# Kernel tuning notes

Measured on AMD Instinct MI355X. Metric: run time of the kernel, lower is better.

## Reference

```python
import jax, jax.numpy as jnp
import numpy as np
import math

B, N, C_IN = 4, 512, 32
K = 3            # Chebyshev order -> K+1 polynomial terms
H = 4            # attention heads
OUT_PER_HEAD = 64
ACT_OUT = OUT_PER_HEAD * H  # concat_heads=True


def _prelu(x, a):
    return jnp.where(x >= 0, x, a * x)


def setup_inputs() -> dict:
    key = jax.random.key(0)
    ks = jax.random.split(key, 10)
    stdv = 1.0 / math.sqrt(ACT_OUT)
    inp = {
        "X_real": jax.random.normal(ks[0], (B, N, C_IN), jnp.float32),
        "X_imag": jax.random.normal(ks[1], (B, N, C_IN), jnp.float32),
        "L_real": jax.random.normal(ks[2], (B, K + 1, N, N), jnp.float32),
        "L_imag": jax.random.normal(ks[3], (B, K + 1, N, N), jnp.float32),
        # Chebyshev complex weights, uniform(-stdv, stdv) as in torch init
        "weight_real": jax.random.uniform(ks[4], (K + 1, C_IN, ACT_OUT), jnp.float32, -stdv, stdv),
        "weight_imag": jax.random.uniform(ks[5], (K + 1, C_IN, ACT_OUT), jnp.float32, -stdv, stdv),
        # CVLinear(2*C_IN -> H) complex weight/bias
        "attn_w_real": jax.random.normal(ks[6], (2 * C_IN, H), jnp.float32) * 0.1,
        "attn_w_imag": jax.random.normal(ks[7], (2 * C_IN, H), jnp.float32) * 0.1,
        "attn_b_real": jnp.zeros((H,), jnp.float32),
        "attn_b_imag": jnp.zeros((H,), jnp.float32),
        # CPReLU slopes (PReLU applied to real/imag parts independently)
        "prelu_a_real": jnp.float32(0.25),
        "prelu_a_imag": jnp.float32(0.25),
        "bias_real": jnp.zeros((1, ACT_OUT), jnp.float32),
        "bias_imag": jnp.zeros((1, ACT_OUT), jnp.float32),
    }
    return inp


def reference(X_real, X_imag, L_real, L_imag, weight_real, weight_imag,
              attn_w_real, attn_w_imag, attn_b_real, attn_b_imag,
              prelu_a_real, prelu_a_imag, bias_real, bias_imag):
    C = X_real.shape[-1]
    K1 = weight_real.shape[0]
    # --- attention scores: complex linear on concat([X_i, X_j]) ---
    # split the 2C weight into the X_i half and the X_j half (same math,
    # avoids materializing the B*N*N*2C pairwise concat tensor)
    W1r, W2r = attn_w_real[:C], attn_w_real[C:]
    W1i, W2i = attn_w_imag[:C], attn_w_imag[C:]
    si_re = X_real @ W1r - X_imag @ W1i   # (B,N,H)
    si_im = X_real @ W1i + X_imag @ W1r
    sj_re = X_real @ W2r - X_imag @ W2i
    sj_im = X_real @ W2i + X_imag @ W2r
    # scores[b,i,j,h]
    sc_re = si_re[:, :, None, :] + sj_re[:, None, :, :] + attn_b_real
    sc_im = si_im[:, :, None, :] + sj_im[:, None, :, :] + attn_b_imag
    # CPReLU: PReLU on real/imag independently
    sc_re = _prelu(sc_re, prelu_a_real)
    sc_im = _prelu(sc_im, prelu_a_imag)
    # adjacency mask from |L_real| summed over the K+1 polynomial terms
    mask = (jnp.abs(L_real).sum(axis=1) > 1e-9)[..., None]  # (B,N,N,1)
    NEG = jnp.float32(-1e9)
    re_m = jnp.where(mask, sc_re, NEG)
    im_m = jnp.where(mask, sc_im, NEG)
    attn = jax.nn.softmax(re_m * re_m + im_m * im_m, axis=2)  # softmax over j, (B,N,N,H)
    # --- complex Chebyshev propagation: (L*attn) @ X, per k, per head ---
    lre_xr = jnp.einsum('bknj,bnjh,bjc->bknch', L_real, attn, X_real)
    lim_xi = jnp.einsum('bknj,bnjh,bjc->bknch', L_imag, attn, X_imag)
    lre_xi = jnp.einsum('bknj,bnjh,bjc->bknch', L_real, attn, X_imag)
    lim_xr = jnp.einsum('bknj,bnjh,bjc->bknch', L_imag, attn, X_real)
    LXr = lre_xr - lim_xi
    LXi = lre_xi + lim_xr
    # per-head complex weights: (K+1, C, P, H), out index = p*H + h
    Wr = weight_real.reshape(K1, C, OUT_PER_HEAD, H)
    Wi = weight_imag.reshape(K1, C, OUT_PER_HEAD, H)
    Yre = jnp.einsum('bknch,kcph->bnph', LXr, Wr) - jnp.einsum('bknch,kcph->bnph', LXi, Wi)
    Yim = jnp.einsum('bknch,kcph->bnph', LXr, Wi) + jnp.einsum('bknch,kcph->bnph', LXi, Wr)
    Bsz, Nn = X_real.shape[:2]
    out_re = Yre.reshape(Bsz, Nn, -1) + bias_real
    out_im = Yim.reshape(Bsz, Nn, -1) + bias_imag
    return (out_re, out_im)
```

## Files before the change

kernel.cpp:

```cpp
#include <hip/hip_runtime.h>
#include <hip/hip_bf16.h>

#define BB 4
#define NN 512
#define CC 32
#define KK 4
#define HH 4
#define AOUT 256

#define WS_SI_F   0
#define WS_SII_F  (BB*NN*HH)
#define WS_SJR_F  (2*BB*NN*HH)
#define WS_SJI_F  (3*BB*NN*HH)
#define XT_BASE   131072
#define LX_BASE   393216
#define BRE_BASE  4587520
#define BIM_BASE  4718592

typedef __attribute__((ext_vector_type(8))) short bf16x8;
typedef __attribute__((ext_vector_type(4))) float f32x4;

__device__ __forceinline__ ushort f2bfu(float f){
    union { __hip_bfloat16 h; ushort u; } cv;
    cv.h = __float2bfloat16(f);
    return cv.u;
}
__device__ __forceinline__ short f2bfs(float f){ return (short)f2bfu(f); }
__device__ __forceinline__ float bfu2f(unsigned int u){ return __uint_as_float(u << 16); }

__global__ __launch_bounds__(256) void prep_kernel(
    const float* __restrict__ Xr, const float* __restrict__ Xi,
    const float* __restrict__ AWr, const float* __restrict__ AWi,
    const float* __restrict__ Wr, const float* __restrict__ Wi,
    float* __restrict__ ws, char* __restrict__ wsB)
{
    const int blk = blockIdx.x;
    const int t = threadIdx.x;

    if (blk < 8) {
        int idx = blk*256 + t;
        const float* xr = Xr + (size_t)idx * CC;
        const float* xi = Xi + (size_t)idx * CC;
        float sir[HH] = {0,0,0,0}, sii[HH] = {0,0,0,0};
        float sjr[HH] = {0,0,0,0}, sji[HH] = {0,0,0,0};
        for (int c = 0; c < CC; ++c) {
            float xrc = xr[c], xic = xi[c];
            const float* w1r = AWr + c*HH;
            const float* w1i = AWi + c*HH;
            const float* w2r = AWr + (CC + c)*HH;
            const float* w2i = AWi + (CC + c)*HH;
            #pragma unroll
            for (int h = 0; h < HH; ++h) {
                sir[h] = fmaf(xrc, w1r[h], fmaf(-xic, w1i[h], sir[h]));
                sii[h] = fmaf(xrc, w1i[h], fmaf( xic, w1r[h], sii[h]));
                sjr[h] = fmaf(xrc, w2r[h], fmaf(-xic, w2i[h], sjr[h]));
                sji[h] = fmaf(xrc, w2i[h], fmaf( xic, w2r[h], sji[h]));
            }
        }
        #pragma unroll
        for (int h = 0; h < HH; ++h) {
            ws[WS_SI_F  + idx*HH + h] = sir[h];
            ws[WS_SII_F + idx*HH + h] = sii[h];
            ws[WS_SJR_F + idx*HH + h] = sjr[h];
            ws[WS_SJI_F + idx*HH + h] = sji[h];
        }
    } else if (blk < 40) {
        int bid = (blk - 8)*4 + (t >> 6);
        int part = bid >> 6, b = (bid >> 4) & 3, jb = bid & 15;
        const float* X = part ? Xi : Xr;
        int lane = t & 63;
        int c = lane & 31, jh = lane >> 5;

        unsigned int w[8];
        #pragma unroll
        for (int q = 0; q < 8; ++q) {
            int ji = jh*16 + q*2;
            float f0 = X[((size_t)b*NN + jb*32 + ji  )*CC + c];
            float f1 = X[((size_t)b*NN + jb*32 + ji+1)*CC + c];
            w[q] = (unsigned int)f2bfu(f0) | ((unsigned int)f2bfu(f1) << 16);
        }
        char* tile = wsB + XT_BASE + (((size_t)(part*4 + b)*16 + jb) * 2048);
        uint4* dst = (uint4*)(tile + c*64 + jh*32);
        dst[0] = make_uint4(w[0], w[1], w[2], w[3]);
        dst[1] = make_uint4(w[4], w[5], w[6], w[7]);
    } else {
        int idx = (blk - 40)*256 + t;
        int l  = idx & 63;
        int s  = (idx >> 6) & 7;
        int Nt = (idx >> 9) & 3;
        int h  = idx >> 11;
        int p = Nt*16 + (l & 15), o = p*4 + h;
        int e8 = (l >> 4) * 8;
        unsigned int re_w[4], im_w[4];
        #pragma unroll
        for (int q = 0; q < 4; ++q) {
            unsigned int rw = 0, iw = 0;
            #pragma unroll
            for (int half = 0; half < 2; ++half) {
                int kpos = s*32 + e8 + q*2 + half;
                int ri = kpos >> 7, kk = (kpos >> 5) & 3, c = kpos & 31;
                float wr = Wr[(size_t)(kk*CC + c)*AOUT + o];
                float wi = Wi[(size_t)(kk*CC + c)*AOUT + o];
                unsigned int vre = f2bfu(ri ? -wi : wr);
                unsigned int vim = f2bfu(ri ?  wr : wi);
                rw |= vre << (16*half);
                iw |= vim << (16*half);
            }
            re_w[q] = rw; im_w[q] = iw;
        }
        size_t fo = ((size_t)((h*4 + Nt)*8 + s))*1024 + (size_t)l*16;
        *(uint4*)(wsB + BRE_BASE + fo) = make_uint4(re_w[0], re_w[1], re_w[2], re_w[3]);
        *(uint4*)(wsB + BIM_BASE + fo) = make_uint4(im_w[0], im_w[1], im_w[2], im_w[3]);
    }
}

__global__ __launch_bounds__(128) void cheb_main_kernel(
    const float* __restrict__ Lr_g, const float* __restrict__ Li_g,
    const float* __restrict__ abr, const float* __restrict__ abi,
    const float* __restrict__ par, const float* __restrict__ pai,
    const float* __restrict__ ws, char* __restrict__ wsB)
{
    __shared__ ushort Lf[8][528];
    __shared__ float awf[HH][520];
    __shared__ float wredm[2][HH];
    __shared__ float wreds[2][HH];

    const int bn = blockIdx.x;
    const int b = bn >> 9;
    const int n = bn & (NN - 1);
    const int t = threadIdx.x;
    const int l = t & 63;
    const int w = t >> 6;
    const int jw = 4*t;

    const float4 si_r4 = *(const float4*)(ws + WS_SI_F  + bn*HH);
    const float4 si_i4 = *(const float4*)(ws + WS_SII_F + bn*HH);
    float4 sjr[4], sji[4];
    #pragma unroll
    for (int e = 0; e < 4; ++e) {
        sjr[e] = *(const float4*)(ws + WS_SJR_F + ((size_t)b*NN + jw + e)*HH);
        sji[e] = *(const float4*)(ws + WS_SJI_F + ((size_t)b*NN + jw + e)*HH);
    }
    const float a_r = par[0], a_i = pai[0];

    float am4[4] = {0.f,0.f,0.f,0.f};
    #pragma unroll
    for (int it = 0; it < 8; ++it) {
        const float* src = (it & 4) ? Li_g : Lr_g;
        size_t goff = (((size_t)b*KK + (it & 3))*NN + n)*NN + jw;
        float4 v = *(const float4*)(src + goff);
        if (it < 4) {
            am4[0] += fabsf(v.x); am4[1] += fabsf(v.y);
            am4[2] += fabsf(v.z); am4[3] += fabsf(v.w);
        }
        ushort4 u;
        u.x = f2bfu(v.x); u.y = f2bfu(v.y); u.z = f2bfu(v.z); u.w = f2bfu(v.w);
        *(ushort4*)&Lf[it][jw] = u;
    }

    float sir[HH], sii[HH];
    #pragma unroll
    for (int h = 0; h < HH; ++h) {
        sir[h] = ((const float*)&si_r4)[h] + abr[h];
        sii[h] = ((const float*)&si_i4)[h] + abi[h];
    }
    float v[4][HH];
    float pmax[HH] = {-INFINITY, -INFINITY, -INFINITY, -INFINITY};
    #pragma unroll
    for (int e = 0; e < 4; ++e) {
        bool msk = am4[e] > 1e-9f;
        const float* sjrp = (const float*)&sjr[e];
        const float* sjip = (const float*)&sji[e];
        #pragma unroll
        for (int h = 0; h < HH; ++h) {
            float sr = sir[h] + sjrp[h];
            sr = sr >= 0.f ? sr : a_r * sr;
            float sv = sii[h] + sjip[h];
            sv = sv >= 0.f ? sv : a_i * sv;
            float val;
            if (msk) val = sr*sr + sv*sv;
            else { const float NEG = -1e9f; val = NEG*NEG + NEG*NEG; }
            v[e][h] = val;
            pmax[h] = fmaxf(pmax[h], val);
        }
    }
    #pragma unroll
    for (int h = 0; h < HH; ++h) {
        #pragma unroll
        for (int off = 32; off > 0; off >>= 1)
            pmax[h] = fmaxf(pmax[h], __shfl_xor(pmax[h], off));
    }
    if (l == 0) { wredm[w][0]=pmax[0]; wredm[w][1]=pmax[1]; wredm[w][2]=pmax[2]; wredm[w][3]=pmax[3]; }
    __syncthreads();

    float hm[HH];
    #pragma unroll
    for (int h = 0; h < HH; ++h) hm[h] = fmaxf(wredm[0][h], wredm[1][h]);

    float psum[HH];
    #pragma unroll
    for (int h = 0; h < HH; ++h) {
        float4 ev;
        ev.x = __expf(v[0][h] - hm[h]);
        ev.y = __expf(v[1][h] - hm[h]);
        ev.z = __expf(v[2][h] - hm[h]);
        ev.w = __expf(v[3][h] - hm[h]);
        *(float4*)&awf[h][jw] = ev;
        psum[h] = (ev.x + ev.y) + (ev.z + ev.w);
    }
    #pragma unroll
    for (int h = 0; h < HH; ++h) {
        #pragma unroll
        for (int off = 32; off > 0; off >>= 1)
            psum[h] += __shfl_xor(psum[h], off);
    }
    if (l == 0) { wreds[w][0]=psum[0]; wreds[w][1]=psum[1]; wreds[w][2]=psum[2]; wreds[w][3]=psum[3]; }
    __syncthreads();

    float inv[HH];
    #pragma unroll
    for (int h = 0; h < HH; ++h) inv[h] = 1.0f / (wreds[0][h] + wreds[1][h]);

    const int r_a = l & 15;
    const int jg  = l >> 4;
    const int k_a = r_a >> 2, h_a = r_a & 3;

    f32x4 acc[8];
    #pragma unroll
    for (int a = 0; a < 8; ++a) acc[a] = (f32x4){0.f,0.f,0.f,0.f};

    const char* xtR = wsB + XT_BASE + ((size_t)(0*4 + b)*16 + w*8)*2048;
    const char* xtI = wsB + XT_BASE + ((size_t)(4   + b)*16 + w*8)*2048;
    const int bofs = (l & 15)*64 + jg*16;

#define LOAD_STEP(s, BR0,BR1,BI0,BI1, LR8,LI8, AW0,AW1) do {                  \
        const int j0_ = w*256 + (s)*32 + jg*8;                                \
        BR0 = *(const bf16x8*)(xtR + (s)*2048 +        bofs);                 \
        BR1 = *(const bf16x8*)(xtR + (s)*2048 + 1024 + bofs);                 \
        BI0 = *(const bf16x8*)(xtI + (s)*2048 +        bofs);                 \
        BI1 = *(const bf16x8*)(xtI + (s)*2048 + 1024 + bofs);                 \
        LR8 = *(const bf16x8*)&Lf[k_a][j0_];                                  \
        LI8 = *(const bf16x8*)&Lf[4 + k_a][j0_];                              \
        AW0 = *(const float4*)&awf[h_a][j0_];                                 \
        AW1 = *(const float4*)&awf[h_a][j0_ + 4];                             \
    } while (0)

#define COMP_STEP(BR0,BR1,BI0,BI1, LR8,LI8, AW0,AW1) do {                     \
        float aww_[8];                                                        \
        *(float4*)&aww_[0] = AW0; *(float4*)&aww_[4] = AW1;                   \
        bf16x8 Ar_, Ai_;                                                      \
        _Pragma("unroll")                                                     \
        for (int e_ = 0; e_ < 8; ++e_) {                                      \
            Ar_[e_] = f2bfs(bfu2f((ushort)LR8[e_]) * aww_[e_]);               \
            Ai_[e_] = f2bfs(bfu2f((ushort)LI8[e_]) * aww_[e_]);               \
        }                                                                     \
        acc[0] = __builtin_amdgcn_mfma_f32_16x16x32_bf16(Ar_, BR0, acc[0],0,0,0); \
        acc[1] = __builtin_amdgcn_mfma_f32_16x16x32_bf16(Ar_, BR1, acc[1],0,0,0); \
        acc[2] = __builtin_amdgcn_mfma_f32_16x16x32_bf16(Ai_, BI0, acc[2],0,0,0); \
        acc[3] = __builtin_amdgcn_mfma_f32_16x16x32_bf16(Ai_, BI1, acc[3],0,0,0); \
        acc[4] = __builtin_amdgcn_mfma_f32_16x16x32_bf16(Ar_, BI0, acc[4],0,0,0); \
        acc[5] = __builtin_amdgcn_mfma_f32_16x16x32_bf16(Ar_, BI1, acc[5],0,0,0); \
        acc[6] = __builtin_amdgcn_mfma_f32_16x16x32_bf16(Ai_, BR0, acc[6],0,0,0); \
        acc[7] = __builtin_amdgcn_mfma_f32_16x16x32_bf16(Ai_, BR1, acc[7],0,0,0); \
    } while (0)

    {
        bf16x8 pBr0,pBr1,pBi0,pBi1,pLr,pLi; float4 pA0,pA1;
        bf16x8 qBr0,qBr1,qBi0,qBi1,qLr,qLi; float4 qA0,qA1;
        LOAD_STEP(0, pBr0,pBr1,pBi0,pBi1, pLr,pLi, pA0,pA1);
        LOAD_STEP(1, qBr0,qBr1,qBi0,qBi1, qLr,qLi, qA0,qA1);
        COMP_STEP(pBr0,pBr1,pBi0,pBi1, pLr,pLi, pA0,pA1);
        LOAD_STEP(2, pBr0,pBr1,pBi0,pBi1, pLr,pLi, pA0,pA1);
        COMP_STEP(qBr0,qBr1,qBi0,qBi1, qLr,qLi, qA0,qA1);
        LOAD_STEP(3, qBr0,qBr1,qBi0,qBi1, qLr,qLi, qA0,qA1);
        COMP_STEP(pBr0,pBr1,pBi0,pBi1, pLr,pLi, pA0,pA1);
        LOAD_STEP(4, pBr0,pBr1,pBi0,pBi1, pLr,pLi, pA0,pA1);
        COMP_STEP(qBr0,qBr1,qBi0,qBi1, qLr,qLi, qA0,qA1);
        LOAD_STEP(5, qBr0,qBr1,qBi0,qBi1, qLr,qLi, qA0,qA1);
        COMP_STEP(pBr0,pBr1,pBi0,pBi1, pLr,pLi, pA0,pA1);
        LOAD_STEP(6, pBr0,pBr1,pBi0,pBi1, pLr,pLi, pA0,pA1);
        COMP_STEP(qBr0,qBr1,qBi0,qBi1, qLr,qLi, qA0,qA1);
        LOAD_STEP(7, qBr0,qBr1,qBi0,qBi1, qLr,qLi, qA0,qA1);
        COMP_STEP(pBr0,pBr1,pBi0,pBi1, pLr,pLi, pA0,pA1);
        COMP_STEP(qBr0,qBr1,qBi0,qBi1, qLr,qLi, qA0,qA1);
    }
#undef LOAD_STEP
#undef COMP_STEP

    __syncthreads();

    float* pbuf = &awf[0][0];
    if (w == 1) {
        #pragma unroll
        for (int a = 0; a < 8; ++a)
            #pragma unroll
            for (int r = 0; r < 4; ++r)
                pbuf[(a*4 + r)*64 + l] = acc[a][r];
    }
    __syncthreads();
    if (w == 0) {
        const int kk = l >> 4, lc = l & 15;
        #pragma unroll
        for (int a = 0; a < 8; ++a)
            #pragma unroll
            for (int r = 0; r < 4; ++r)
                acc[a][r] += pbuf[(a*4 + r)*64 + l];
        char* lxp = wsB + LX_BASE + (size_t)bn*2048;
        #pragma unroll
        for (int ct = 0; ct < 2; ++ct) {
            const int c = ct*16 + lc;
            #pragma unroll
            for (int r = 0; r < 4; ++r) {
                float iv = inv[r];
                float vr = (acc[0+ct][r] - acc[2+ct][r]) * iv;
                float vi = (acc[4+ct][r] + acc[6+ct][r]) * iv;
                *(ushort*)(lxp + r*512 +       kk*64 + c*2) = f2bfu(vr);
                *(ushort*)(lxp + r*512 + 256 + kk*64 + c*2) = f2bfu(vi);
            }
        }
    }
}

__global__ __launch_bounds__(256) void out_gemm_kernel(
    const char* __restrict__ wsB,
    const float* __restrict__ bsr, const float* __restrict__ bsi,
    float* __restrict__ out)
{
    const int Mtile = blockIdx.x >> 2;
    const int Nt    = blockIdx.x & 3;
    const int t = threadIdx.x, l = t & 63, h = t >> 6;

    const char* abase = wsB + LX_BASE + ((size_t)(Mtile*16 + (l & 15)))*2048
                        + h*512 + (l >> 4)*16;
    f32x4 are = (f32x4){0.f,0.f,0.f,0.f};
    f32x4 aim = (f32x4){0.f,0.f,0.f,0.f};
    const size_t fbase = ((size_t)((h*4 + Nt)*8))*1024 + (size_t)l*16;
    const char* bre = wsB + BRE_BASE + fbase;
    const char* bim = wsB + BIM_BASE + fbase;
    #pragma unroll
    for (int s = 0; s < 8; ++s) {
        bf16x8 Af = *(const bf16x8*)(abase + s*64);
        bf16x8 Br = *(const bf16x8*)(bre + s*1024);
        bf16x8 Bi = *(const bf16x8*)(bim + s*1024);
        are = __builtin_amdgcn_mfma_f32_16x16x32_bf16(Af, Br, are, 0, 0, 0);
        aim = __builtin_amdgcn_mfma_f32_16x16x32_bf16(Af, Bi, aim, 0, 0, 0);
    }
    const int p = Nt*16 + (l & 15), o = p*4 + h;
    const float vbr = bsr[o], vbi = bsi[o];
    #pragma unroll
    for (int r = 0; r < 4; ++r) {
        int bn = Mtile*16 + (l >> 4)*4 + r;
        out[(size_t)bn*AOUT + o] = are[r] + vbr;
        out[(size_t)BB*NN*AOUT + (size_t)bn*AOUT + o] = aim[r] + vbi;
    }
}

extern "C" void kernel_launch(void* const* d_in, const int* in_sizes, int n_in,
                              void* d_out, int out_size, void* d_ws, size_t ws_size,
                              hipStream_t stream)
{
    const float* Xr  = (const float*)d_in[0];
    const float* Xi  = (const float*)d_in[1];
    const float* Lr  = (const float*)d_in[2];
    const float* Li  = (const float*)d_in[3];
    const float* Wr  = (const float*)d_in[4];
    const float* Wi  = (const float*)d_in[5];
    const float* AWr = (const float*)d_in[6];
    const float* AWi = (const float*)d_in[7];
    const float* abr = (const float*)d_in[8];
    const float* abi = (const float*)d_in[9];
    const float* par = (const float*)d_in[10];
    const float* pai = (const float*)d_in[11];
    const float* bsr = (const float*)d_in[12];
    const float* bsi = (const float*)d_in[13];
    float* ws  = (float*)d_ws;
    char*  wsB = (char*)d_ws;
    float* out = (float*)d_out;

    hipLaunchKernelGGL(prep_kernel, dim3(72), dim3(256), 0, stream,
                       Xr, Xi, AWr, AWi, Wr, Wi, ws, wsB);
    hipLaunchKernelGGL(cheb_main_kernel, dim3(BB*NN), dim3(128), 0, stream,
                       Lr, Li, abr, abi, par, pai, ws, wsB);
    hipLaunchKernelGGL(out_gemm_kernel, dim3(512), dim3(256), 0, stream,
                       wsB, bsr, bsi, out);
}
```

Before: 32.06 us.

## Prefetch X tiles early, split reduction across waves, parallelize attention score prep

The prep kernel's attention-score stage now uses four threads per row, each covering 8 channels with vectorised loads, and combines the partial sums with lane shuffles. This adds more blocks and cuts the serial 32-channel loop. The main kernel issues the first two X-tile loads before the L loads and softmax so their latency is hidden, and uses a three-buffer rotation of B fragments. L and attention-weight LDS reads move into the compute step, and launch bounds now request 4 blocks per CU. The final cross-wave reduction and store are split so each wave finishes half the channels, which balances the epilogue at the cost of more live registers.

Measured after the change: 32.84 us. 2.5% more time.

```diff
diff --git a/kernel.cpp b/kernel.cpp
--- a/kernel.cpp
+++ b/kernel.cpp
@@ -37,35 +37,57 @@
     const int blk = blockIdx.x;
     const int t = threadIdx.x;
 
-    if (blk < 8) {
-        int idx = blk*256 + t;
-        const float* xr = Xr + (size_t)idx * CC;
-        const float* xi = Xi + (size_t)idx * CC;
+    if (blk < 32) {
+        const int row = blk*64 + (t >> 2);
+        const int q = t & 3;
+        const float* xr = Xr + (size_t)row*CC + q*8;
+        const float* xi = Xi + (size_t)row*CC + q*8;
+        float4 xr4[2], xi4[2];
+        xr4[0] = *(const float4*)xr;  xr4[1] = *(const float4*)(xr + 4);
+        xi4[0] = *(const float4*)xi;  xi4[1] = *(const float4*)(xi + 4);
+
         float sir[HH] = {0,0,0,0}, sii[HH] = {0,0,0,0};
         float sjr[HH] = {0,0,0,0}, sji[HH] = {0,0,0,0};
-        for (int c = 0; c < CC; ++c) {
-            float xrc = xr[c], xic = xi[c];
-            const float* w1r = AWr + c*HH;
-            const float* w1i = AWi + c*HH;
-            const float* w2r = AWr + (CC + c)*HH;
-            const float* w2i = AWi + (CC + c)*HH;
+        #pragma unroll
+        for (int e = 0; e < 8; ++e) {
+            float xrc = ((const float*)&xr4[e>>2])[e & 3];
+            float xic = ((const float*)&xi4[e>>2])[e & 3];
+            int c = q*8 + e;
+            float4 w1r = *(const float4*)(AWr + c*HH);
+            float4 w1i = *(const float4*)(AWi + c*HH);
+            float4 w2r = *(const float4*)(AWr + (CC + c)*HH);
+            float4 w2i = *(const float4*)(AWi + (CC + c)*HH);
             #pragma unroll
             for (int h = 0; h < HH; ++h) {
-                sir[h] = fmaf(xrc, w1r[h], fmaf(-xic, w1i[h], sir[h]));
-                sii[h] = fmaf(xrc, w1i[h], fmaf( xic, w1r[h], sii[h]));
-                sjr[h] = fmaf(xrc, w2r[h], fmaf(-xic, w2i[h], sjr[h]));
-                sji[h] = fmaf(xrc, w2i[h], fmaf( xic, w2r[h], sji[h]));
+                float r1 = ((const float*)&w1r)[h], i1 = ((const float*)&w1i)[h];
+                float r2 = ((const float*)&w2r)[h], i2 = ((const float*)&w2i)[h];
+                sir[h] = fmaf(xrc, r1, fmaf(-xic, i1, sir[h]));
+                sii[h] = fmaf(xrc, i1, fmaf( xic, r1, sii[h]));
+                sjr[h] = fmaf(xrc, r2, fmaf(-xic, i2, sjr[h]));
+                sji[h] = fmaf(xrc, i2, fmaf( xic, r2, sji[h]));
             }
         }
+        float A[HH], Bv[HH];
         #pragma unroll
         for (int h = 0; h < HH; ++h) {
-            ws[WS_SI_F  + idx*HH + h] = sir[h];
-            ws[WS_SII_F + idx*HH + h] = sii[h];
-            ws[WS_SJR_F + idx*HH + h] = sjr[h];
-            ws[WS_SJI_F + idx*HH + h] = sji[h];
-        }
-    } else if (blk < 40) {
-        int bid = (blk - 8)*4 + (t >> 6);
+            float sendA = (q & 1) ? sir[h] : sii[h];
+            float keepA = (q & 1) ? sii[h] : sir[h];
+            A[h] = keepA + __shfl_xor(sendA, 1);
+            float sendB = (q & 1) ? sjr[h] : sji[h];
+            float keepB = (q & 1) ? sji[h] : sjr[h];
+            Bv[h] = keepB + __shfl_xor(sendB, 1);
+        }
+        float tot[HH];
+        #pragma unroll
+        for (int h = 0; h < HH; ++h) {
+            float send = (q & 2) ? A[h] : Bv[h];
+            float keep = (q & 2) ? Bv[h] : A[h];
+            tot[h] = keep + __shfl_xor(send, 2);
+        }
+        float4 v = make_float4(tot[0], tot[1], tot[2], tot[3]);
+        *(float4*)(ws + (size_t)q*(BB*NN*HH) + (size_t)row*HH) = v;
+    } else if (blk < 64) {
+        int bid = (blk - 32)*4 + (t >> 6);
         int part = bid >> 6, b = (bid >> 4) & 3, jb = bid & 15;
         const float* X = part ? Xi : Xr;
         int lane = t & 63;
@@ -73,18 +95,18 @@
 
         unsigned int w[8];
         #pragma unroll
-        for (int q = 0; q < 8; ++q) {
-            int ji = jh*16 + q*2;
+        for (int qq = 0; qq < 8; ++qq) {
+            int ji = jh*16 + qq*2;
             float f0 = X[((size_t)b*NN + jb*32 + ji  )*CC + c];
             float f1 = X[((size_t)b*NN + jb*32 + ji+1)*CC + c];
-            w[q] = (unsigned int)f2bfu(f0) | ((unsigned int)f2bfu(f1) << 16);
+            w[qq] = (unsigned int)f2bfu(f0) | ((unsigned int)f2bfu(f1) << 16);
         }
         char* tile = wsB + XT_BASE + (((size_t)(part*4 + b)*16 + jb) * 2048);
         uint4* dst = (uint4*)(tile + c*64 + jh*32);
         dst[0] = make_uint4(w[0], w[1], w[2], w[3]);
         dst[1] = make_uint4(w[4], w[5], w[6], w[7]);
     } else {
-        int idx = (blk - 40)*256 + t;
+        int idx = (blk - 64)*256 + t;
         int l  = idx & 63;
         int s  = (idx >> 6) & 7;
         int Nt = (idx >> 9) & 3;
@@ -93,11 +115,11 @@
         int e8 = (l >> 4) * 8;
         unsigned int re_w[4], im_w[4];
         #pragma unroll
-        for (int q = 0; q < 4; ++q) {
+        for (int qq = 0; qq < 4; ++qq) {
             unsigned int rw = 0, iw = 0;
             #pragma unroll
             for (int half = 0; half < 2; ++half) {
-                int kpos = s*32 + e8 + q*2 + half;
+                int kpos = s*32 + e8 + qq*2 + half;
                 int ri = kpos >> 7, kk = (kpos >> 5) & 3, c = kpos & 31;
                 float wr = Wr[(size_t)(kk*CC + c)*AOUT + o];
                 float wi = Wi[(size_t)(kk*CC + c)*AOUT + o];
@@ -106,7 +128,7 @@
                 rw |= vre << (16*half);
                 iw |= vim << (16*half);
             }
-            re_w[q] = rw; im_w[q] = iw;
+            re_w[qq] = rw; im_w[qq] = iw;
         }
         size_t fo = ((size_t)((h*4 + Nt)*8 + s))*1024 + (size_t)l*16;
         *(uint4*)(wsB + BRE_BASE + fo) = make_uint4(re_w[0], re_w[1], re_w[2], re_w[3]);
@@ -114,7 +136,7 @@
     }
 }
 
-__global__ __launch_bounds__(128) void cheb_main_kernel(
+__global__ __launch_bounds__(128, 4) void cheb_main_kernel(
     const float* __restrict__ Lr_g, const float* __restrict__ Li_g,
     const float* __restrict__ abr, const float* __restrict__ abi,
     const float* __restrict__ par, const float* __restrict__ pai,
@@ -142,6 +164,22 @@
         sji[e] = *(const float4*)(ws + WS_SJI_F + ((size_t)b*NN + jw + e)*HH);
     }
     const float a_r = par[0], a_i = pai[0];
+
+    const char* xtR = wsB + XT_BASE + ((size_t)(0*4 + b)*16 + w*8)*2048;
+    const char* xtI = wsB + XT_BASE + ((size_t)(4   + b)*16 + w*8)*2048;
+    const int jg  = l >> 4;
+    const int bofs = (l & 15)*64 + jg*16;
+
+#define LB(s, BR0,BR1,BI0,BI1) do {                                           \
+        BR0 = *(const bf16x8*)(xtR + (s)*2048 +        bofs);                 \
+        BR1 = *(const bf16x8*)(xtR + (s)*2048 + 1024 + bofs);                 \
+        BI0 = *(const bf16x8*)(xtI + (s)*2048 +        bofs);                 \
+        BI1 = *(const bf16x8*)(xtI + (s)*2048 + 1024 + bofs);                 \
+    } while (0)
+
+    bf16x8 pR0,pR1,pI0,pI1, qR0,qR1,qI0,qI1, rR0,rR1,rI0,rI1;
+    LB(0, pR0,pR1,pI0,pI1);
+    LB(1, qR0,qR1,qI0,qI1);
 
     float am4[4] = {0.f,0.f,0.f,0.f};
     #pragma unroll
@@ -222,32 +260,19 @@
     for (int h = 0; h < HH; ++h) inv[h] = 1.0f / (wreds[0][h] + wreds[1][h]);
 
     const int r_a = l & 15;
-    const int jg  = l >> 4;
     const int k_a = r_a >> 2, h_a = r_a & 3;
 
     f32x4 acc[8];
     #pragma unroll
     for (int a = 0; a < 8; ++a) acc[a] = (f32x4){0.f,0.f,0.f,0.f};
 
-    const char* xtR = wsB + XT_BASE + ((size_t)(0*4 + b)*16 + w*8)*2048;
-    const char* xtI = wsB + XT_BASE + ((size_t)(4   + b)*16 + w*8)*2048;
-    const int bofs = (l & 15)*64 + jg*16;
-
-#define LOAD_STEP(s, BR0,BR1,BI0,BI1, LR8,LI8, AW0,AW1) do {                  \
+#define COMP(s, BR0,BR1,BI0,BI1) do {                                         \
         const int j0_ = w*256 + (s)*32 + jg*8;                                \
-        BR0 = *(const bf16x8*)(xtR + (s)*2048 +        bofs);                 \
-        BR1 = *(const bf16x8*)(xtR + (s)*2048 + 1024 + bofs);                 \
-        BI0 = *(const bf16x8*)(xtI + (s)*2048 +        bofs);                 \
-        BI1 = *(const bf16x8*)(xtI + (s)*2048 + 1024 + bofs);                 \
-        LR8 = *(const bf16x8*)&Lf[k_a][j0_];                                  \
-        LI8 = *(const bf16x8*)&Lf[4 + k_a][j0_];                              \
-        AW0 = *(const float4*)&awf[h_a][j0_];                                 \
-        AW1 = *(const float4*)&awf[h_a][j0_ + 4];                             \
-    } while (0)
-
-#define COMP_STEP(BR0,BR1,BI0,BI1, LR8,LI8, AW0,AW1) do {                     \
+        bf16x8 LR8 = *(const bf16x8*)&Lf[k_a][j0_];                           \
+        bf16x8 LI8 = *(const bf16x8*)&Lf[4 + k_a][j0_];                       \
         float aww_[8];                                                        \
-        *(float4*)&aww_[0] = AW0; *(float4*)&aww_[4] = AW1;                   \
+        *(float4*)&aww_[0] = *(const float4*)&awf[h_a][j0_];                  \
+        *(float4*)&aww_[4] = *(const float4*)&awf[h_a][j0_ + 4];              \
         bf16x8 Ar_, Ai_;                                                      \
         _Pragma("unroll")                                                     \
         for (int e_ = 0; e_ < 8; ++e_) {                                      \
@@ -264,59 +289,65 @@
         acc[7] = __builtin_amdgcn_mfma_f32_16x16x32_bf16(Ai_, BR1, acc[7],0,0,0); \
     } while (0)
 
-    {
-        bf16x8 pBr0,pBr1,pBi0,pBi1,pLr,pLi; float4 pA0,pA1;
-        bf16x8 qBr0,qBr1,qBi0,qBi1,qLr,qLi; float4 qA0,qA1;
-        LOAD_STEP(0, pBr0,pBr1,pBi0,pBi1, pLr,pLi, pA0,pA1);
-        LOAD_STEP(1, qBr0,qBr1,qBi0,qBi1, qLr,qLi, qA0,qA1);
-        COMP_STEP(pBr0,pBr1,pBi0,pBi1, pLr,pLi, pA0,pA1);
-        LOAD_STEP(2, pBr0,pBr1,pBi0,pBi1, pLr,pLi, pA0,pA1);
-        COMP_STEP(qBr0,qBr1,qBi0,qBi1, qLr,qLi, qA0,qA1);
-        LOAD_STEP(3, qBr0,qBr1,qBi0,qBi1, qLr,qLi, qA0,qA1);
-        COMP_STEP(pBr0,pBr1,pBi0,pBi1, pLr,pLi, pA0,pA1);
-        LOAD_STEP(4, pBr0,pBr1,pBi0,pBi1, pLr,pLi, pA0,pA1);
-        COMP_STEP(qBr0,qBr1,qBi0,qBi1, qLr,qLi, qA0,qA1);
-        LOAD_STEP(5, qBr0,qBr1,qBi0,qBi1, qLr,qLi, qA0,qA1);
-        COMP_STEP(pBr0,pBr1,pBi0,pBi1, pLr,pLi, pA0,pA1);
-        LOAD_STEP(6, pBr0,pBr1,pBi0,pBi1, pLr,pLi, pA0,pA1);
-        COMP_STEP(qBr0,qBr1,qBi0,qBi1, qLr,qLi, qA0,qA1);
-        LOAD_STEP(7, qBr0,qBr1,qBi0,qBi1, qLr,qLi, qA0,qA1);
-        COMP_STEP(pBr0,pBr1,pBi0,pBi1, pLr,pLi, pA0,pA1);
-        COMP_STEP(qBr0,qBr1,qBi0,qBi1, qLr,qLi, qA0,qA1);
-    }
-#undef LOAD_STEP
-#undef COMP_STEP
+    LB(2, rR0,rR1,rI0,rI1);  COMP(0, pR0,pR1,pI0,pI1);
+    LB(3, pR0,pR1,pI0,pI1);  COMP(1, qR0,qR1,qI0,qI1);
+    LB(4, qR0,qR1,qI0,qI1);  COMP(2, rR0,rR1,rI0,rI1);
+    LB(5, rR0,rR1,rI0,rI1);  COMP(3, pR0,pR1,pI0,pI1);
+    LB(6, pR0,pR1,pI0,pI1);  COMP(4, qR0,qR1,qI0,qI1);
+    LB(7, qR0,qR1,qI0,qI1);  COMP(5, rR0,rR1,rI0,rI1);
+    COMP(6, pR0,pR1,pI0,pI1);
+    COMP(7, qR0,qR1,qI0,qI1);
+#undef LB
+#undef COMP
 
     __syncthreads();
 
     float* pbuf = &awf[0][0];
     if (w == 1) {
         #pragma unroll
-        for (int a = 0; a < 8; ++a)
+        for (int ae = 0; ae < 4; ++ae)
             #pragma unroll
             for (int r = 0; r < 4; ++r)
-                pbuf[(a*4 + r)*64 + l] = acc[a][r];
+                pbuf[(ae*4 + r)*64 + l] = acc[2*ae][r];
+    } else {
+        #pragma unroll
+        for (int ao = 0; ao < 4; ++ao)
+            #pragma unroll
+            for (int r = 0; r < 4; ++r)
+                pbuf[1024 + (ao*4 + r)*64 + l] = acc[2*ao + 1][r];
     }
     __syncthreads();
+
+    const int kk = l >> 4, lc = l & 15;
+    char* lxp = wsB + LX_BASE + (size_t)bn*2048;
     if (w == 0) {
-        const int kk = l >> 4, lc = l & 15;
-        #pragma unroll
-        for (int a = 0; a < 8; ++a)
+        #pragma unroll
+        for (int ae = 0; ae < 4; ++ae)
             #pragma unroll
             for (int r = 0; r < 4; ++r)
-                acc[a][r] += pbuf[(a*4 + r)*64 + l];
-        char* lxp = wsB + LX_BASE + (size_t)bn*2048;
-        #pragma unroll
-        for (int ct = 0; ct < 2; ++ct) {
-            const int c = ct*16 + lc;
-            #pragma unroll
-            for (int r = 0; r < 4; ++r) {
-                float iv = inv[r];
-                float vr = (acc[0+ct][r] - acc[2+ct][r]) * iv;
-                float vi = (acc[4+ct][r] + acc[6+ct][r]) * iv;
-                *(ushort*)(lxp + r*512 +       kk*64 + c*2) = f2bfu(vr);
-                *(ushort*)(lxp + r*512 + 256 + kk*64 + c*2) = f2bfu(vi);
-            }
+                acc[2*ae][r] += pbuf[(ae*4 + r)*64 + l];
+        #pragma unroll
+        for (int r = 0; r < 4; ++r) {
+            float iv = inv[r];
+            float vr = (acc[0][r] - acc[2][r]) * iv;
+            float vi = (acc[4][r] + acc[6][r]) * iv;
+            *(ushort*)(lxp + r*512 +       kk*64 + lc*2) = f2bfu(vr);
+            *(ushort*)(lxp + r*512 + 256 + kk*64 + lc*2) = f2bfu(vi);
+        }
+    } else {
+        #pragma unroll
+        for (int ao = 0; ao < 4; ++ao)
+            #pragma unroll
+            for (int r = 0; r < 4; ++r)
+                acc[2*ao + 1][r] += pbuf[1024 + (ao*4 + r)*64 + l];
+        const int c = 16 + lc;
+        #pragma unroll
+        for (int r = 0; r < 4; ++r) {
+            float iv = inv[r];
+            float vr = (acc[1][r] - acc[3][r]) * iv;
+            float vi = (acc[5][r] + acc[7][r]) * iv;
+            *(ushort*)(lxp + r*512 +       kk*64 + c*2) = f2bfu(vr);
+            *(ushort*)(lxp + r*512 + 256 + kk*64 + c*2) = f2bfu(vi);
         }
     }
 }
@@ -377,7 +408,7 @@
     char*  wsB = (char*)d_ws;
     float* out = (float*)d_out;
 
-    hipLaunchKernelGGL(prep_kernel, dim3(72), dim3(256), 0, stream,
+    hipLaunchKernelGGL(prep_kernel, dim3(96), dim3(256), 0, stream,
                        Xr, Xi, AWr, AWi, Wr, Wi, ws, wsB);
     hipLaunchKernelGGL(cheb_main_kernel, dim3(BB*NN), dim3(128), 0, stream,
                        Lr, Li, abr, abi, par, pai, ws, wsB);
```

## Drop cross-wave LDS reduction in main kernel; fold partial sums into output GEMM

Applied to the files above, without the earlier changes.

The main kernel no longer reduces the two waves' partial accumulators through shared memory with two barriers. Each wave now writes its own bf16 partial LX slab, and the output GEMM adds the two partials by issuing twice as many MFMAs over both slabs. The prep kernel's attention-score part is also reworked so four threads per row each handle 8 channels with vector loads and combine results via shuffles. The cost is twice the LX workspace traffic and extra MFMAs in the output GEMM, plus one more bf16 rounding on the split partial sums.

After: 38.32 us. +19.5%, slower.

```diff
diff --git a/kernel.cpp b/kernel.cpp
--- a/kernel.cpp
+++ b/kernel.cpp
@@ -14,8 +14,8 @@
 #define WS_SJI_F  (3*BB*NN*HH)
 #define XT_BASE   131072
 #define LX_BASE   393216
-#define BRE_BASE  4587520
-#define BIM_BASE  4718592
+#define BRE_BASE  (393216 + 2048*4096)
+#define BIM_BASE  (BRE_BASE + 131072)
 
 typedef __attribute__((ext_vector_type(8))) short bf16x8;
 typedef __attribute__((ext_vector_type(4))) float f32x4;
@@ -37,35 +37,57 @@
     const int blk = blockIdx.x;
     const int t = threadIdx.x;
 
-    if (blk < 8) {
-        int idx = blk*256 + t;
-        const float* xr = Xr + (size_t)idx * CC;
-        const float* xi = Xi + (size_t)idx * CC;
+    if (blk < 32) {
+        const int row = blk*64 + (t >> 2);
+        const int q = t & 3;
+        const float* xr = Xr + (size_t)row*CC + q*8;
+        const float* xi = Xi + (size_t)row*CC + q*8;
+        float4 xr4[2], xi4[2];
+        xr4[0] = *(const float4*)xr;  xr4[1] = *(const float4*)(xr + 4);
+        xi4[0] = *(const float4*)xi;  xi4[1] = *(const float4*)(xi + 4);
+
         float sir[HH] = {0,0,0,0}, sii[HH] = {0,0,0,0};
         float sjr[HH] = {0,0,0,0}, sji[HH] = {0,0,0,0};
-        for (int c = 0; c < CC; ++c) {
-            float xrc = xr[c], xic = xi[c];
-            const float* w1r = AWr + c*HH;
-            const float* w1i = AWi + c*HH;
-            const float* w2r = AWr + (CC + c)*HH;
-            const float* w2i = AWi + (CC + c)*HH;
+        #pragma unroll
+        for (int e = 0; e < 8; ++e) {
+            float xrc = ((const float*)&xr4[e>>2])[e & 3];
+            float xic = ((const float*)&xi4[e>>2])[e & 3];
+            int c = q*8 + e;
+            float4 w1r = *(const float4*)(AWr + c*HH);
+            float4 w1i = *(const float4*)(AWi + c*HH);
+            float4 w2r = *(const float4*)(AWr + (CC + c)*HH);
+            float4 w2i = *(const float4*)(AWi + (CC + c)*HH);
             #pragma unroll
             for (int h = 0; h < HH; ++h) {
-                sir[h] = fmaf(xrc, w1r[h], fmaf(-xic, w1i[h], sir[h]));
-                sii[h] = fmaf(xrc, w1i[h], fmaf( xic, w1r[h], sii[h]));
-                sjr[h] = fmaf(xrc, w2r[h], fmaf(-xic, w2i[h], sjr[h]));
-                sji[h] = fmaf(xrc, w2i[h], fmaf( xic, w2r[h], sji[h]));
+                float r1 = ((const float*)&w1r)[h], i1 = ((const float*)&w1i)[h];
+                float r2 = ((const float*)&w2r)[h], i2 = ((const float*)&w2i)[h];
+                sir[h] = fmaf(xrc, r1, fmaf(-xic, i1, sir[h]));
+                sii[h] = fmaf(xrc, i1, fmaf( xic, r1, sii[h]));
+                sjr[h] = fmaf(xrc, r2, fmaf(-xic, i2, sjr[h]));
+                sji[h] = fmaf(xrc, i2, fmaf( xic, r2, sji[h]));
             }
         }
+        float A[HH], Bv[HH];
         #pragma unroll
         for (int h = 0; h < HH; ++h) {
-            ws[WS_SI_F  + idx*HH + h] = sir[h];
-            ws[WS_SII_F + idx*HH + h] = sii[h];
-            ws[WS_SJR_F + idx*HH + h] = sjr[h];
-            ws[WS_SJI_F + idx*HH + h] = sji[h];
-        }
-    } else if (blk < 40) {
-        int bid = (blk - 8)*4 + (t >> 6);
+            float sendA = (q & 1) ? sir[h] : sii[h];
+            float keepA = (q & 1) ? sii[h] : sir[h];
+            A[h] = keepA + __shfl_xor(sendA, 1);
+            float sendB = (q & 1) ? sjr[h] : sji[h];
+            float keepB = (q & 1) ? sji[h] : sjr[h];
+            Bv[h] = keepB + __shfl_xor(sendB, 1);
+        }
+        float tot[HH];
+        #pragma unroll
+        for (int h = 0; h < HH; ++h) {
+            float send = (q & 2) ? A[h] : Bv[h];
+            float keep = (q & 2) ? Bv[h] : A[h];
+            tot[h] = keep + __shfl_xor(send, 2);
+        }
+        float4 v = make_float4(tot[0], tot[1], tot[2], tot[3]);
+        *(float4*)(ws + (size_t)q*(BB*NN*HH) + (size_t)row*HH) = v;
+    } else if (blk < 64) {
+        int bid = (blk - 32)*4 + (t >> 6);
         int part = bid >> 6, b = (bid >> 4) & 3, jb = bid & 15;
         const float* X = part ? Xi : Xr;
         int lane = t & 63;
@@ -73,18 +95,18 @@
 
         unsigned int w[8];
         #pragma unroll
-        for (int q = 0; q < 8; ++q) {
-            int ji = jh*16 + q*2;
+        for (int qq = 0; qq < 8; ++qq) {
+            int ji = jh*16 + qq*2;
             float f0 = X[((size_t)b*NN + jb*32 + ji  )*CC + c];
             float f1 = X[((size_t)b*NN + jb*32 + ji+1)*CC + c];
-            w[q] = (unsigned int)f2bfu(f0) | ((unsigned int)f2bfu(f1) << 16);
+            w[qq] = (unsigned int)f2bfu(f0) | ((unsigned int)f2bfu(f1) << 16);
         }
         char* tile = wsB + XT_BASE + (((size_t)(part*4 + b)*16 + jb) * 2048);
         uint4* dst = (uint4*)(tile + c*64 + jh*32);
         dst[0] = make_uint4(w[0], w[1], w[2], w[3]);
         dst[1] = make_uint4(w[4], w[5], w[6], w[7]);
     } else {
-        int idx = (blk - 40)*256 + t;
+        int idx = (blk - 64)*256 + t;
         int l  = idx & 63;
         int s  = (idx >> 6) & 7;
         int Nt = (idx >> 9) & 3;
@@ -93,11 +115,11 @@
         int e8 = (l >> 4) * 8;
         unsigned int re_w[4], im_w[4];
         #pragma unroll
-        for (int q = 0; q < 4; ++q) {
+        for (int qq = 0; qq < 4; ++qq) {
             unsigned int rw = 0, iw = 0;
             #pragma unroll
             for (int half = 0; half < 2; ++half) {
-                int kpos = s*32 + e8 + q*2 + half;
+                int kpos = s*32 + e8 + qq*2 + half;
                 int ri = kpos >> 7, kk = (kpos >> 5) & 3, c = kpos & 31;
                 float wr = Wr[(size_t)(kk*CC + c)*AOUT + o];
                 float wi = Wi[(size_t)(kk*CC + c)*AOUT + o];
@@ -106,7 +128,7 @@
                 rw |= vre << (16*half);
                 iw |= vim << (16*half);
             }
-            re_w[q] = rw; im_w[q] = iw;
+            re_w[qq] = rw; im_w[qq] = iw;
         }
         size_t fo = ((size_t)((h*4 + Nt)*8 + s))*1024 + (size_t)l*16;
         *(uint4*)(wsB + BRE_BASE + fo) = make_uint4(re_w[0], re_w[1], re_w[2], re_w[3]);
@@ -287,36 +309,18 @@
 #undef LOAD_STEP
 #undef COMP_STEP
 
-    __syncthreads();
-
-    float* pbuf = &awf[0][0];
-    if (w == 1) {
-        #pragma unroll
-        for (int a = 0; a < 8; ++a)
-            #pragma unroll
-            for (int r = 0; r < 4; ++r)
-                pbuf[(a*4 + r)*64 + l] = acc[a][r];
-    }
-    __syncthreads();
-    if (w == 0) {
-        const int kk = l >> 4, lc = l & 15;
-        #pragma unroll
-        for (int a = 0; a < 8; ++a)
-            #pragma unroll
-            for (int r = 0; r < 4; ++r)
-                acc[a][r] += pbuf[(a*4 + r)*64 + l];
-        char* lxp = wsB + LX_BASE + (size_t)bn*2048;
-        #pragma unroll
-        for (int ct = 0; ct < 2; ++ct) {
-            const int c = ct*16 + lc;
-            #pragma unroll
-            for (int r = 0; r < 4; ++r) {
-                float iv = inv[r];
-                float vr = (acc[0+ct][r] - acc[2+ct][r]) * iv;
-                float vi = (acc[4+ct][r] + acc[6+ct][r]) * iv;
-                *(ushort*)(lxp + r*512 +       kk*64 + c*2) = f2bfu(vr);
-                *(ushort*)(lxp + r*512 + 256 + kk*64 + c*2) = f2bfu(vi);
-            }
+    const int kk = l >> 4, lc = l & 15;
+    char* lxp = wsB + LX_BASE + (size_t)bn*4096 + (size_t)w*2048;
+    #pragma unroll
+    for (int ct = 0; ct < 2; ++ct) {
+        const int c = ct*16 + lc;
+        #pragma unroll
+        for (int r = 0; r < 4; ++r) {
+            float iv = inv[r];
+            float vr = (acc[0+ct][r] - acc[2+ct][r]) * iv;
+            float vi = (acc[4+ct][r] + acc[6+ct][r]) * iv;
+            *(ushort*)(lxp + r*512 +       kk*64 + c*2) = f2bfu(vr);
+            *(ushort*)(lxp + r*512 + 256 + kk*64 + c*2) = f2bfu(vi);
         }
     }
 }
@@ -330,8 +334,9 @@
     const int Nt    = blockIdx.x & 3;
     const int t = threadIdx.x, l = t & 63, h = t >> 6;
 
-    const char* abase = wsB + LX_BASE + ((size_t)(Mtile*16 + (l & 15)))*2048
-                        + h*512 + (l >> 4)*16;
+    const char* abase0 = wsB + LX_BASE + ((size_t)(Mtile*16 + (l & 15)))*4096
+                         + h*512 + (l >> 4)*16;
+    const char* abase1 = abase0 + 2048;
     f32x4 are = (f32x4){0.f,0.f,0.f,0.f};
     f32x4 aim = (f32x4){0.f,0.f,0.f,0.f};
     const size_t fbase = ((size_t)((h*4 + Nt)*8))*1024 + (size_t)l*16;
@@ -339,11 +344,14 @@
     const char* bim = wsB + BIM_BASE + fbase;
     #pragma unroll
     for (int s = 0; s < 8; ++s) {
-        bf16x8 Af = *(const bf16x8*)(abase + s*64);
-        bf16x8 Br = *(const bf16x8*)(bre + s*1024);
-        bf16x8 Bi = *(const bf16x8*)(bim + s*1024);
-        are = __builtin_amdgcn_mfma_f32_16x16x32_bf16(Af, Br, are, 0, 0, 0);
-        aim = __builtin_amdgcn_mfma_f32_16x16x32_bf16(Af, Bi, aim, 0, 0, 0);
+        bf16x8 Af0 = *(const bf16x8*)(abase0 + s*64);
+        bf16x8 Af1 = *(const bf16x8*)(abase1 + s*64);
+        bf16x8 Br  = *(const bf16x8*)(bre + s*1024);
+        bf16x8 Bi  = *(const bf16x8*)(bim + s*1024);
+        are = __builtin_amdgcn_mfma_f32_16x16x32_bf16(Af0, Br, are, 0, 0, 0);
+        are = __builtin_amdgcn_mfma_f32_16x16x32_bf16(Af1, Br, are, 0, 0, 0);
+        aim = __builtin_amdgcn_mfma_f32_16x16x32_bf16(Af0, Bi, aim, 0, 0, 0);
+        aim = __builtin_amdgcn_mfma_f32_16x16x32_bf16(Af1, Bi, aim, 0, 0, 0);
     }
     const int p = Nt*16 + (l & 15), o = p*4 + h;
     const float vbr = bsr[o], vbi = bsi[o];
@@ -377,7 +385,7 @@
     char*  wsB = (char*)d_ws;
     float* out = (float*)d_out;
 
-    hipLaunchKernelGGL(prep_kernel, dim3(72), dim3(256), 0, stream,
+    hipLaunchKernelGGL(prep_kernel, dim3(96), dim3(256), 0, stream,
                        Xr, Xi, AWr, AWi, Wr, Wi, ws, wsB);
     hipLaunchKernelGGL(cheb_main_kernel, dim3(BB*NN), dim3(128), 0, stream,
                        Lr, Li, abr, abi, par, pai, ws, wsB);
```
